# Kernel tuning notes

Hardware: AMD Instinct MI355X
Metric: run time of the kernel (lower is better)

Reference implementation:

```python
import jax, jax.numpy as jnp
import numpy as np

EMBED = 64
HEADS = 2
HDIM = EMBED // HEADS  # 32
IN_FEAT = 256
NODES = 3


def _lin(x, W, b=None):
    y = x @ W.T
    return y + b if b is not None else y


def setup_inputs() -> dict:
    key = jax.random.key(0)
    ks = jax.random.split(key, 24)
    B = 131072
    s = 0.05
    inp = {
        "spatial": jax.random.normal(ks[0], (B, IN_FEAT), jnp.float32),
        "genomic": jax.random.normal(ks[1], (B, IN_FEAT), jnp.float32),
        "temporal": jax.random.normal(ks[2], (B, IN_FEAT), jnp.float32),
        "adj_matrix": jnp.ones((B, NODES, NODES), jnp.float32),
        # modality projections (Linear(256,64))
        "Wsp": jax.random.normal(ks[3], (EMBED, IN_FEAT)) * s,
        "bsp": jnp.zeros((EMBED,)),
        "Wge": jax.random.normal(ks[4], (EMBED, IN_FEAT)) * s,
        "bge": jnp.zeros((EMBED,)),
        "Wtm": jax.random.normal(ks[5], (EMBED, IN_FEAT)) * s,
        "btm": jnp.zeros((EMBED,)),
        # GAT: W Linear(64,64,no bias), attention Linear(2*head_dim=64 -> 1, no bias)
        "gat_W": jax.random.normal(ks[6], (EMBED, EMBED)) * s,
        "gat_a": jax.random.normal(ks[7], (2 * HDIM,)) * s,
        # MultiheadAttention(64, 2)
        "in_w": jax.random.normal(ks[8], (3 * EMBED, EMBED)) * s,
        "in_b": jnp.zeros((3 * EMBED,)),
        "out_w": jax.random.normal(ks[9], (EMBED, EMBED)) * s,
        "out_b": jnp.zeros((EMBED,)),
        # LayerNorm(64)
        "ln_g": jnp.ones((EMBED,)),
        "ln_b": jnp.zeros((EMBED,)),
        # predictor 64->32->16->2
        "p1_w": jax.random.normal(ks[10], (32, EMBED)) * s,
        "p1_b": jnp.zeros((32,)),
        "p2_w": jax.random.normal(ks[11], (16, 32)) * s,
        "p2_b": jnp.zeros((16,)),
        "p3_w": jax.random.normal(ks[12], (2, 16)) * s,
        "p3_b": jnp.zeros((2,)),
    }
    return inp


def reference(spatial, genomic, temporal, adj_matrix,
              Wsp, bsp, Wge, bge, Wtm, btm,
              gat_W, gat_a, in_w, in_b, out_w, out_b,
              ln_g, ln_b, p1_w, p1_b, p2_w, p2_b, p3_w, p3_b):
    # Dropout layers are identity in eval mode.
    B = spatial.shape[0]
    sp = jax.nn.relu(_lin(spatial, Wsp, bsp))   # [B, 64]
    ge = jax.nn.relu(_lin(genomic, Wge, bge))
    tm = jax.nn.relu(_lin(temporal, Wtm, btm))
    x = jnp.stack([sp, ge, tm], axis=1)          # [B, 3, 64]

    # ---- GAT layer (dense attention over 3 nodes, 2 heads) ----
    h = _lin(x, gat_W).reshape(B, NODES, HEADS, HDIM)  # [B,3,H,D]
    # a . concat(h_i, h_j) decomposes into a1.h_i + a2.h_j
    e_i = jnp.einsum('bnhd,d->bnh', h, gat_a[:HDIM])
    e_j = jnp.einsum('bnhd,d->bnh', h, gat_a[HDIM:])
    e = e_i[:, :, None, :] + e_j[:, None, :, :]        # [B,3,3,H]
    e = jnp.where(e > 0, e, 0.2 * e)                    # LeakyReLU(0.2)
    e = jnp.where(adj_matrix[..., None] == 0, -1e9, e)
    alpha = jax.nn.softmax(e, axis=2)                   # softmax over j
    h_out = jnp.einsum('bijh,bjhd->bihd', alpha, h).reshape(B, NODES, EMBED)
    gat_pooled = h_out.mean(axis=1)                     # [B, 64]

    # ---- Cross-modal MHA + residual LayerNorm ----
    qkv = _lin(x, in_w, in_b)                           # [B,3,192]
    q, k, v = jnp.split(qkv, 3, axis=-1)
    def heads(t):
        return t.reshape(B, NODES, HEADS, HDIM).transpose(0, 2, 1, 3)
    q, k, v = heads(q), heads(k), heads(v)              # [B,H,3,D]
    sc = jnp.einsum('bhqd,bhkd->bhqk', q, k) / jnp.sqrt(jnp.float32(HDIM))
    attn = jax.nn.softmax(sc, axis=-1)
    o = jnp.einsum('bhqk,bhkd->bhqd', attn, v).transpose(0, 2, 1, 3).reshape(B, NODES, EMBED)
    attn_out = _lin(o, out_w, out_b)
    y = x + attn_out
    mu = y.mean(-1, keepdims=True)
    var = ((y - mu) ** 2).mean(-1, keepdims=True)
    y = (y - mu) / jnp.sqrt(var + 1e-5) * ln_g + ln_b
    cross_modal = y.mean(axis=1)                        # [B, 64]

    # ---- Predictor ----
    combined = gat_pooled + cross_modal
    z = jax.nn.relu(_lin(combined, p1_w, p1_b))
    z = jax.nn.relu(_lin(z, p2_w, p2_b))
    out = _lin(z, p3_w, p3_b)                           # [B, 2]
    return out[:, 0], out[:, 1]
```

## Files before the change

kernel.cpp:

```cpp
#include <hip/hip_runtime.h>

typedef __attribute__((ext_vector_type(8))) short v8s;
typedef __attribute__((ext_vector_type(4))) float v4f;

#define MFMA16(a, b, c) __builtin_amdgcn_mfma_f32_16x16x32_bf16((a), (b), (c), 0, 0, 0)

__device__ __forceinline__ short f2bf(float f) {
    unsigned u = __float_as_uint(f);
    u += 0x7FFFu + ((u >> 16) & 1u);
    return (short)(u >> 16);
}
__device__ __forceinline__ float bf2f(short s) {
    return __uint_as_float(((unsigned)(unsigned short)s) << 16);
}
__device__ __forceinline__ float bfly16(float v) {
#pragma unroll
    for (int m = 1; m < 16; m <<= 1) v += __shfl_xor(v, m);
    return v;
}

__global__ void giman_prep(const float* __restrict__ Wsp, const float* __restrict__ Wge,
                           const float* __restrict__ Wtm, const float* __restrict__ gatW,
                           const float* __restrict__ inw, const float* __restrict__ outw,
                           const float* __restrict__ p1w, const float* __restrict__ p2w,
                           const float* __restrict__ in_b, const float* __restrict__ out_b,
                           short* __restrict__ ws) {
    int idx = blockIdx.x * 256 + threadIdx.x;
    if (idx < 72192) {
        int j = idx & 7, l = (idx >> 3) & 63;
        int lr = l & 15, lc = ((l >> 4) << 3) + j;
        float val;
        if (idx < 49152) {
            const float* W; int off;
            if (idx < 16384)      { W = Wsp; off = idx; }
            else if (idx < 32768) { W = Wge; off = idx - 16384; }
            else                  { W = Wtm; off = idx - 32768; }
            int t = off >> 9, kk = t & 7, nb = t >> 3;
            val = W[(nb * 16 + lr) * 256 + kk * 32 + lc];
        } else if (idx < 53248) {
            int t = (idx - 49152) >> 9, kk = t & 1, nb = t >> 1;
            val = gatW[(nb * 16 + lr) * 64 + kk * 32 + lc];
        } else if (idx < 61440) {
            int t = (idx - 53248) >> 9, kk = t & 1, nb = t >> 1;
            val = inw[(nb * 16 + lr) * 64 + kk * 32 + lc];
        } else if (idx < 69632) {
            int t = (idx - 61440) >> 9, kk = t & 1, nbh = t >> 1;
            int h = nbh >> 2, nb = nbh & 3;
            int r = nb * 16 + lr, c = kk * 32 + lc;
            float s = 0.f;
            for (int k = 0; k < 32; ++k)
                s += outw[r * 64 + h * 32 + k] * inw[(128 + h * 32 + k) * 64 + c];
            val = s;
        } else if (idx < 71680) {
            int t = (idx - 69632) >> 9, kk = t & 1, nb = t >> 1;
            val = p1w[(nb * 16 + lr) * 64 + kk * 32 + lc];
        } else {
            val = p2w[lr * 32 + lc];
        }
        ws[idx] = f2bf(val);
    } else if (idx < 72256) {
        int r = idx - 72192;
        float s = out_b[r];
        for (int k = 0; k < 64; ++k) s += outw[r * 64 + 128 + k] * in_b[128 + k];
        ((float*)(ws + 72192))[r] = s;
    }
}

__global__ __launch_bounds__(256)
void giman_main(const float* __restrict__ spatial, const float* __restrict__ genomic,
                const float* __restrict__ temporal, const float* __restrict__ adj,
                const short* __restrict__ wf,
                const float* __restrict__ bsp, const float* __restrict__ bge,
                const float* __restrict__ btm, const float* __restrict__ gat_a,
                const float* __restrict__ in_b, const float* __restrict__ ln_g,
                const float* __restrict__ ln_b, const float* __restrict__ p1b,
                const float* __restrict__ p2b, const float* __restrict__ p3w,
                const float* __restrict__ p3bb,
                float* __restrict__ dout, int Btot)
{
    __shared__ __align__(16) short x_lds[4][48][72];
    __shared__ __align__(16) short c_lds[4][16][72];
    __shared__ __align__(16) float a_lds[4][148];

    const int wv   = threadIdx.x >> 6;
    const int lane = threadIdx.x & 63;
    const int lq   = lane & 15;
    const int lg   = lane >> 4;
    const int s0   = blockIdx.x * 64 + wv * 16;
    if (s0 + 16 > Btot) return;

    short (*xw)[72] = x_lds[wv];

    if (lane < 36)
        *(float4*)&a_lds[wv][lane * 4] = *(const float4*)(adj + (size_t)s0 * 9 + lane * 4);

    const float* cbp = (const float*)(wf + 72192);
    float a1v[4], a2v[4], cbv[4], lgv[4], lbv[4], ibv[8];
#pragma unroll
    for (int nb = 0; nb < 4; ++nb) {
        int c = nb * 16 + lq;
        a1v[nb] = gat_a[c & 31];
        a2v[nb] = gat_a[32 + (c & 31)];
        cbv[nb] = cbp[c];
        lgv[nb] = ln_g[c];
        lbv[nb] = ln_b[c];
    }
#pragma unroll
    for (int nb = 0; nb < 8; ++nb) ibv[nb] = in_b[nb * 16 + lq];
    const float inv3 = 1.f / 3.f;

    {
        const float* Xs[3] = {spatial, genomic, temporal};
        const float* Bs[3] = {bsp, bge, btm};
#pragma unroll
        for (int m = 0; m < 3; ++m) {
            const float* X = Xs[m] + (size_t)(s0 + lq) * 256 + lg * 8;
            const v8s* bwf = (const v8s*)(wf + m * 16384);
            v4f acc[4];
#pragma unroll
            for (int nb = 0; nb < 4; ++nb) acc[nb] = (v4f){0.f, 0.f, 0.f, 0.f};
#pragma unroll 4
            for (int kk = 0; kk < 8; ++kk) {
                float4 u = *(const float4*)(X + kk * 32);
                float4 v = *(const float4*)(X + kk * 32 + 4);
                v8s af;
                af[0] = f2bf(u.x); af[1] = f2bf(u.y); af[2] = f2bf(u.z); af[3] = f2bf(u.w);
                af[4] = f2bf(v.x); af[5] = f2bf(v.y); af[6] = f2bf(v.z); af[7] = f2bf(v.w);
#pragma unroll
                for (int nb = 0; nb < 4; ++nb)
                    acc[nb] = MFMA16(af, bwf[(nb * 8 + kk) * 64 + lane], acc[nb]);
            }
#pragma unroll
            for (int nb = 0; nb < 4; ++nb) {
                float bb = Bs[m][nb * 16 + lq];
#pragma unroll
                for (int r = 0; r < 4; ++r) {
                    float v = acc[nb][r] + bb;
                    v = v > 0.f ? v : 0.f;
                    xw[(lg * 4 + r) * 3 + m][nb * 16 + lq] = f2bf(v);
                }
            }
        }
    }

    const v8s* gwf = (const v8s*)(wf + 49152);
    const v8s* qkf = (const v8s*)(wf + 53248);
    const v8s* uf  = (const v8s*)(wf + 61440);

#pragma unroll 1
    for (int t = 0; t < 4; ++t) {
        int rn = lq & 3; rn = (rn == 3) ? 2 : rn;
        const short* xrp = xw[(t * 4 + (lq >> 2)) * 3 + rn];
        v8s xa0 = *(const v8s*)(xrp + lg * 8);
        v8s xa1 = *(const v8s*)(xrp + 32 + lg * 8);

        float gp[4];
        {
            v4f hacc[4];
#pragma unroll
            for (int nb = 0; nb < 4; ++nb) {
                v4f a = (v4f){0.f, 0.f, 0.f, 0.f};
                a = MFMA16(xa0, gwf[(nb * 2 + 0) * 64 + lane], a);
                a = MFMA16(xa1, gwf[(nb * 2 + 1) * 64 + lane], a);
                hacc[nb] = a;
            }
            float ei[3][2] = {}, ej[3][2] = {};
#pragma unroll
            for (int nb = 0; nb < 4; ++nb) {
                int h = nb >> 1;
#pragma unroll
                for (int n = 0; n < 3; ++n) {
                    ei[n][h] += hacc[nb][n] * a1v[nb];
                    ej[n][h] += hacc[nb][n] * a2v[nb];
                }
            }
#pragma unroll
            for (int n = 0; n < 3; ++n)
#pragma unroll
                for (int h = 0; h < 2; ++h) { ei[n][h] = bfly16(ei[n][h]); ej[n][h] = bfly16(ej[n][h]); }

            const float* amp = &a_lds[wv][(t * 4 + lg) * 9];
            float wj0[2] = {}, wj1[2] = {}, wj2[2] = {};
#pragma unroll
            for (int h = 0; h < 2; ++h)
#pragma unroll
                for (int i = 0; i < 3; ++i) {
                    float e0 = ei[i][h] + ej[0][h]; e0 = e0 > 0.f ? e0 : 0.2f * e0; if (amp[i * 3 + 0] == 0.f) e0 = -1e9f;
                    float e1 = ei[i][h] + ej[1][h]; e1 = e1 > 0.f ? e1 : 0.2f * e1; if (amp[i * 3 + 1] == 0.f) e1 = -1e9f;
                    float e2 = ei[i][h] + ej[2][h]; e2 = e2 > 0.f ? e2 : 0.2f * e2; if (amp[i * 3 + 2] == 0.f) e2 = -1e9f;
                    float mx = fmaxf(e0, fmaxf(e1, e2));
                    float q0 = __expf(e0 - mx), q1 = __expf(e1 - mx), q2 = __expf(e2 - mx);
                    float inv = 1.f / (q0 + q1 + q2);
                    wj0[h] += q0 * inv; wj1[h] += q1 * inv; wj2[h] += q2 * inv;
                }
#pragma unroll
            for (int nb = 0; nb < 4; ++nb) {
                int h = nb >> 1;
                gp[nb] = (wj0[h] * hacc[nb][0] + wj1[h] * hacc[nb][1] + wj2[h] * hacc[nb][2]) * inv3;
            }
        }

        float al[2][9];
#pragma unroll
        for (int h = 0; h < 2; ++h) {
            v4f q0, q1, k0, k1;
            {
                float b0 = ibv[2 * h], b1 = ibv[2 * h + 1];
                float b2 = ibv[4 + 2 * h], b3 = ibv[5 + 2 * h];
                q0 = (v4f){b0, b0, b0, b0};
                q1 = (v4f){b1, b1, b1, b1};
                k0 = (v4f){b2, b2, b2, b2};
                k1 = (v4f){b3, b3, b3, b3};
            }
            q0 = MFMA16(xa0, qkf[((2 * h) * 2 + 0) * 64 + lane], q0);
            q0 = MFMA16(xa1, qkf[((2 * h) * 2 + 1) * 64 + lane], q0);
            q1 = MFMA16(xa0, qkf[((2 * h + 1) * 2 + 0) * 64 + lane], q1);
            q1 = MFMA16(xa1, qkf[((2 * h + 1) * 2 + 1) * 64 + lane], q1);
            k0 = MFMA16(xa0, qkf[((4 + 2 * h) * 2 + 0) * 64 + lane], k0);
            k0 = MFMA16(xa1, qkf[((4 + 2 * h) * 2 + 1) * 64 + lane], k0);
            k1 = MFMA16(xa0, qkf[((5 + 2 * h) * 2 + 0) * 64 + lane], k1);
            k1 = MFMA16(xa1, qkf[((5 + 2 * h) * 2 + 1) * 64 + lane], k1);

            float s_[9];
#pragma unroll
            for (int i = 0; i < 3; ++i)
#pragma unroll
                for (int j = 0; j < 3; ++j)
                    s_[i * 3 + j] = bfly16(q0[i] * k0[j] + q1[i] * k1[j]);
#pragma unroll
            for (int i = 0; i < 3; ++i) {
                float e0 = s_[i * 3 + 0] * 0.17677669529663687f;
                float e1 = s_[i * 3 + 1] * 0.17677669529663687f;
                float e2 = s_[i * 3 + 2] * 0.17677669529663687f;
                float mx = fmaxf(e0, fmaxf(e1, e2));
                float w0 = __expf(e0 - mx), w1 = __expf(e1 - mx), w2 = __expf(e2 - mx);
                float inv = 1.f / (w0 + w1 + w2);
                al[h][i * 3 + 0] = w0 * inv;
                al[h][i * 3 + 1] = w1 * inv;
                al[h][i * 3 + 2] = w2 * inv;
            }
        }

        float y[4][3];
#pragma unroll
        for (int nb = 0; nb < 4; ++nb)
#pragma unroll
            for (int r = 0; r < 3; ++r)
                y[nb][r] = bf2f(xw[(t * 4 + lg) * 3 + r][nb * 16 + lq]) + cbv[nb];
#pragma unroll
        for (int h = 0; h < 2; ++h)
#pragma unroll
            for (int nb = 0; nb < 4; ++nb) {
                v4f u = (v4f){0.f, 0.f, 0.f, 0.f};
                u = MFMA16(xa0, uf[((h * 4 + nb) * 2 + 0) * 64 + lane], u);
                u = MFMA16(xa1, uf[((h * 4 + nb) * 2 + 1) * 64 + lane], u);
#pragma unroll
                for (int r = 0; r < 3; ++r)
                    y[nb][r] += al[h][r * 3 + 0] * u[0] + al[h][r * 3 + 1] * u[1]
                              + al[h][r * 3 + 2] * u[2];
            }

        float mu[3], rs[3];
#pragma unroll
        for (int r = 0; r < 3; ++r) {
            float sm = y[0][r] + y[1][r] + y[2][r] + y[3][r];
            float sq = y[0][r] * y[0][r] + y[1][r] * y[1][r]
                     + y[2][r] * y[2][r] + y[3][r] * y[3][r];
            sm = bfly16(sm); sq = bfly16(sq);
            float m_ = sm * (1.f / 64.f);
            float var = sq * (1.f / 64.f) - m_ * m_;
            mu[r] = m_;
            rs[r] = rsqrtf(var + 1e-5f);
        }
#pragma unroll
        for (int nb = 0; nb < 4; ++nb) {
            float cm = (y[nb][0] - mu[0]) * rs[0] + (y[nb][1] - mu[1]) * rs[1]
                     + (y[nb][2] - mu[2]) * rs[2];
            float comb = gp[nb] + cm * inv3 * lgv[nb] + lbv[nb];
            c_lds[wv][t * 4 + lg][nb * 16 + lq] = f2bf(comb);
        }
    }

    {
        const v8s* p1f = (const v8s*)(wf + 69632);
        const v8s* p2f = (const v8s*)(wf + 71680);
        short (*zw)[40] = (short (*)[40])(&x_lds[wv][0][0]);
        const short* crp = &c_lds[wv][lq][0];
        v8s ca0 = *(const v8s*)(crp + lg * 8);
        v8s ca1 = *(const v8s*)(crp + 32 + lg * 8);
        const float pb1v0 = p1b[lq], pb1v1 = p1b[16 + lq], pb2v = p2b[lq];
        const float p3w0 = p3w[lq], p3w1 = p3w[16 + lq];
        v4f z1[2];
#pragma unroll
        for (int nb = 0; nb < 2; ++nb) {
            float bb = nb ? pb1v1 : pb1v0;
            v4f a = (v4f){bb, bb, bb, bb};
            a = MFMA16(ca0, p1f[(nb * 2 + 0) * 64 + lane], a);
            a = MFMA16(ca1, p1f[(nb * 2 + 1) * 64 + lane], a);
            z1[nb] = a;
        }
#pragma unroll
        for (int nb = 0; nb < 2; ++nb)
#pragma unroll
            for (int r = 0; r < 4; ++r) {
                float v = z1[nb][r];
                v = v > 0.f ? v : 0.f;
                zw[lg * 4 + r][nb * 16 + lq] = f2bf(v);
            }
        v8s za = *(const v8s*)(&zw[lq][0] + lg * 8);
        v4f z2 = (v4f){pb2v, pb2v, pb2v, pb2v};
        z2 = MFMA16(za, p2f[lane], z2);
        const float p3b0 = p3bb[0], p3b1 = p3bb[1];
#pragma unroll
        for (int r = 0; r < 4; ++r) {
            float v = z2[r];
            v = v > 0.f ? v : 0.f;
            float po0 = bfly16(v * p3w0);
            float po1 = bfly16(v * p3w1);
            if (lq == 0) {
                dout[s0 + lg * 4 + r] = po0 + p3b0;
                dout[Btot + s0 + lg * 4 + r] = po1 + p3b1;
            }
        }
    }
}

extern "C" void kernel_launch(void* const* d_in, const int* in_sizes, int n_in,
                              void* d_out, int out_size, void* d_ws, size_t ws_size,
                              hipStream_t stream) {
    const float* spatial  = (const float*)d_in[0];
    const float* genomic  = (const float*)d_in[1];
    const float* temporal = (const float*)d_in[2];
    const float* adj      = (const float*)d_in[3];
    const float* Wsp = (const float*)d_in[4];
    const float* bsp = (const float*)d_in[5];
    const float* Wge = (const float*)d_in[6];
    const float* bge = (const float*)d_in[7];
    const float* Wtm = (const float*)d_in[8];
    const float* btm = (const float*)d_in[9];
    const float* gatW  = (const float*)d_in[10];
    const float* gat_a = (const float*)d_in[11];
    const float* in_w  = (const float*)d_in[12];
    const float* in_b  = (const float*)d_in[13];
    const float* out_w = (const float*)d_in[14];
    const float* out_b = (const float*)d_in[15];
    const float* ln_g  = (const float*)d_in[16];
    const float* ln_b  = (const float*)d_in[17];
    const float* p1w = (const float*)d_in[18];
    const float* p1b = (const float*)d_in[19];
    const float* p2w = (const float*)d_in[20];
    const float* p2b = (const float*)d_in[21];
    const float* p3w = (const float*)d_in[22];
    const float* p3b = (const float*)d_in[23];
    float* out = (float*)d_out;
    const int Btot = in_sizes[0] / 256;

    short* wf = (short*)d_ws;

    giman_prep<<<(72256 + 255) / 256, 256, 0, stream>>>(Wsp, Wge, Wtm, gatW, in_w, out_w,
                                                        p1w, p2w, in_b, out_b, wf);
    giman_main<<<Btot / 64, 256, 0, stream>>>(spatial, genomic, temporal, adj, wf,
                                              bsp, bge, btm, gat_a, in_b,
                                              ln_g, ln_b, p1b, p2b, p3w, p3b,
                                              out, Btot);
}
```

Before: 235.2 us.

## Fold GAT attention vector into weights and compute QK scores via MFMA

Precomputes gat_a·W as an extra MFMA weight block, so the GAT edge logits come out of two MFMAs plus shuffles instead of per-lane FMAs and butterfly reductions. The softmax scale is folded into the Q projection weights and bias. Q and K are staged through LDS and the 3x3 score matrix per head is produced with one MFMA instead of nine butterfly reductions. This adds LDS traffic and extra shared memory per block, which may lower occupancy, and rounds Q/K to bf16 before the score product.

```diff
diff --git a/kernel.cpp b/kernel.cpp
--- a/kernel.cpp
+++ b/kernel.cpp
@@ -4,6 +4,7 @@
 typedef __attribute__((ext_vector_type(4))) float v4f;
 
 #define MFMA16(a, b, c) __builtin_amdgcn_mfma_f32_16x16x32_bf16((a), (b), (c), 0, 0, 0)
+#define SCQ 0.17677669529663687f
 
 __device__ __forceinline__ short f2bf(float f) {
     unsigned u = __float_as_uint(f);
@@ -21,12 +22,13 @@
 
 __global__ void giman_prep(const float* __restrict__ Wsp, const float* __restrict__ Wge,
                            const float* __restrict__ Wtm, const float* __restrict__ gatW,
+                           const float* __restrict__ gat_a,
                            const float* __restrict__ inw, const float* __restrict__ outw,
                            const float* __restrict__ p1w, const float* __restrict__ p2w,
                            const float* __restrict__ in_b, const float* __restrict__ out_b,
                            short* __restrict__ ws) {
     int idx = blockIdx.x * 256 + threadIdx.x;
-    if (idx < 72192) {
+    if (idx < 73216) {
         int j = idx & 7, l = (idx >> 3) & 63;
         int lr = l & 15, lc = ((l >> 4) << 3) + j;
         float val;
@@ -37,32 +39,44 @@
             else                  { W = Wtm; off = idx - 32768; }
             int t = off >> 9, kk = t & 7, nb = t >> 3;
             val = W[(nb * 16 + lr) * 256 + kk * 32 + lc];
-        } else if (idx < 53248) {
+        } else if (idx < 54272) {
             int t = (idx - 49152) >> 9, kk = t & 1, nb = t >> 1;
-            val = gatW[(nb * 16 + lr) * 64 + kk * 32 + lc];
-        } else if (idx < 61440) {
-            int t = (idx - 53248) >> 9, kk = t & 1, nb = t >> 1;
-            val = inw[(nb * 16 + lr) * 64 + kk * 32 + lc];
-        } else if (idx < 69632) {
-            int t = (idx - 61440) >> 9, kk = t & 1, nbh = t >> 1;
+            if (nb < 4) {
+                val = gatW[(nb * 16 + lr) * 64 + kk * 32 + lc];
+            } else {
+                val = 0.f;
+                if (lr < 4) {
+                    int f = kk * 32 + lc;
+                    float s = 0.f;
+                    for (int d = 0; d < 32; ++d)
+                        s += gat_a[(lr >> 1) * 32 + d] * gatW[((lr & 1) * 32 + d) * 64 + f];
+                    val = s;
+                }
+            }
+        } else if (idx < 62464) {
+            int t = (idx - 54272) >> 9, kk = t & 1, nb = t >> 1;
+            int row = nb * 16 + lr;
+            val = inw[row * 64 + kk * 32 + lc] * (row < 64 ? SCQ : 1.f);
+        } else if (idx < 70656) {
+            int t = (idx - 62464) >> 9, kk = t & 1, nbh = t >> 1;
             int h = nbh >> 2, nb = nbh & 3;
             int r = nb * 16 + lr, c = kk * 32 + lc;
             float s = 0.f;
             for (int k = 0; k < 32; ++k)
                 s += outw[r * 64 + h * 32 + k] * inw[(128 + h * 32 + k) * 64 + c];
             val = s;
-        } else if (idx < 71680) {
-            int t = (idx - 69632) >> 9, kk = t & 1, nb = t >> 1;
+        } else if (idx < 72704) {
+            int t = (idx - 70656) >> 9, kk = t & 1, nb = t >> 1;
             val = p1w[(nb * 16 + lr) * 64 + kk * 32 + lc];
         } else {
             val = p2w[lr * 32 + lc];
         }
         ws[idx] = f2bf(val);
-    } else if (idx < 72256) {
-        int r = idx - 72192;
+    } else if (idx < 73280) {
+        int r = idx - 73216;
         float s = out_b[r];
         for (int k = 0; k < 64; ++k) s += outw[r * 64 + 128 + k] * in_b[128 + k];
-        ((float*)(ws + 72192))[r] = s;
+        ((float*)(ws + 73216))[r] = s;
     }
 }
 
@@ -71,7 +85,7 @@
                 const float* __restrict__ temporal, const float* __restrict__ adj,
                 const short* __restrict__ wf,
                 const float* __restrict__ bsp, const float* __restrict__ bge,
-                const float* __restrict__ btm, const float* __restrict__ gat_a,
+                const float* __restrict__ btm,
                 const float* __restrict__ in_b, const float* __restrict__ ln_g,
                 const float* __restrict__ ln_b, const float* __restrict__ p1b,
                 const float* __restrict__ p2b, const float* __restrict__ p3w,
@@ -80,33 +94,43 @@
 {
     __shared__ __align__(16) short x_lds[4][48][72];
     __shared__ __align__(16) short c_lds[4][16][72];
+    __shared__ __align__(16) short q_tr[4][16][72];
+    __shared__ __align__(16) short k_tr[4][16][72];
     __shared__ __align__(16) float a_lds[4][148];
 
     const int wv   = threadIdx.x >> 6;
     const int lane = threadIdx.x & 63;
     const int lq   = lane & 15;
     const int lg   = lane >> 4;
+    const int grpb = lane & 48;
     const int s0   = blockIdx.x * 64 + wv * 16;
     if (s0 + 16 > Btot) return;
 
     short (*xw)[72] = x_lds[wv];
+    short (*qtr)[72] = q_tr[wv];
+    short (*ktr)[72] = k_tr[wv];
 
     if (lane < 36)
         *(float4*)&a_lds[wv][lane * 4] = *(const float4*)(adj + (size_t)s0 * 9 + lane * 4);
 
-    const float* cbp = (const float*)(wf + 72192);
-    float a1v[4], a2v[4], cbv[4], lgv[4], lbv[4], ibv[8];
+#pragma unroll
+    for (int nb = 0; nb < 4; ++nb) {
+        qtr[lg * 4 + 3][nb * 16 + lq] = 0;
+        ktr[lg * 4 + 3][nb * 16 + lq] = 0;
+    }
+
+    const float* cbp = (const float*)(wf + 73216);
+    float cbv[4], lgv[4], lbv[4], ibv[8];
 #pragma unroll
     for (int nb = 0; nb < 4; ++nb) {
         int c = nb * 16 + lq;
-        a1v[nb] = gat_a[c & 31];
-        a2v[nb] = gat_a[32 + (c & 31)];
         cbv[nb] = cbp[c];
         lgv[nb] = ln_g[c];
         lbv[nb] = ln_b[c];
     }
 #pragma unroll
-    for (int nb = 0; nb < 8; ++nb) ibv[nb] = in_b[nb * 16 + lq];
+    for (int nb = 0; nb < 8; ++nb)
+        ibv[nb] = in_b[nb * 16 + lq] * (nb < 4 ? SCQ : 1.f);
     const float inv3 = 1.f / 3.f;
 
     {
@@ -144,8 +168,8 @@
     }
 
     const v8s* gwf = (const v8s*)(wf + 49152);
-    const v8s* qkf = (const v8s*)(wf + 53248);
-    const v8s* uf  = (const v8s*)(wf + 61440);
+    const v8s* qkf = (const v8s*)(wf + 54272);
+    const v8s* uf  = (const v8s*)(wf + 62464);
 
 #pragma unroll 1
     for (int t = 0; t < 4; ++t) {
@@ -164,20 +188,19 @@
                 a = MFMA16(xa1, gwf[(nb * 2 + 1) * 64 + lane], a);
                 hacc[nb] = a;
             }
-            float ei[3][2] = {}, ej[3][2] = {};
-#pragma unroll
-            for (int nb = 0; nb < 4; ++nb) {
-                int h = nb >> 1;
-#pragma unroll
-                for (int n = 0; n < 3; ++n) {
-                    ei[n][h] += hacc[nb][n] * a1v[nb];
-                    ej[n][h] += hacc[nb][n] * a2v[nb];
-                }
-            }
-#pragma unroll
-            for (int n = 0; n < 3; ++n)
-#pragma unroll
-                for (int h = 0; h < 2; ++h) { ei[n][h] = bfly16(ei[n][h]); ej[n][h] = bfly16(ej[n][h]); }
+            v4f eacc = (v4f){0.f, 0.f, 0.f, 0.f};
+            eacc = MFMA16(xa0, gwf[8 * 64 + lane], eacc);
+            eacc = MFMA16(xa1, gwf[9 * 64 + lane], eacc);
+
+            float eiv[3][2], ejv[3][2];
+#pragma unroll
+            for (int r = 0; r < 3; ++r) {
+#pragma unroll
+                for (int h = 0; h < 2; ++h) {
+                    eiv[r][h] = __shfl(eacc[r], grpb + h);
+                    ejv[r][h] = __shfl(eacc[r], grpb + 2 + h);
+                }
+            }
 
             const float* amp = &a_lds[wv][(t * 4 + lg) * 9];
             float wj0[2] = {}, wj1[2] = {}, wj2[2] = {};
@@ -185,9 +208,9 @@
             for (int h = 0; h < 2; ++h)
 #pragma unroll
                 for (int i = 0; i < 3; ++i) {
-                    float e0 = ei[i][h] + ej[0][h]; e0 = e0 > 0.f ? e0 : 0.2f * e0; if (amp[i * 3 + 0] == 0.f) e0 = -1e9f;
-                    float e1 = ei[i][h] + ej[1][h]; e1 = e1 > 0.f ? e1 : 0.2f * e1; if (amp[i * 3 + 1] == 0.f) e1 = -1e9f;
-                    float e2 = ei[i][h] + ej[2][h]; e2 = e2 > 0.f ? e2 : 0.2f * e2; if (amp[i * 3 + 2] == 0.f) e2 = -1e9f;
+                    float e0 = eiv[i][h] + ejv[0][h]; e0 = e0 > 0.f ? e0 : 0.2f * e0; if (amp[i * 3 + 0] == 0.f) e0 = -1e9f;
+                    float e1 = eiv[i][h] + ejv[1][h]; e1 = e1 > 0.f ? e1 : 0.2f * e1; if (amp[i * 3 + 1] == 0.f) e1 = -1e9f;
+                    float e2 = eiv[i][h] + ejv[2][h]; e2 = e2 > 0.f ? e2 : 0.2f * e2; if (amp[i * 3 + 2] == 0.f) e2 = -1e9f;
                     float mx = fmaxf(e0, fmaxf(e1, e2));
                     float q0 = __expf(e0 - mx), q1 = __expf(e1 - mx), q2 = __expf(e2 - mx);
                     float inv = 1.f / (q0 + q1 + q2);
@@ -200,44 +223,58 @@
             }
         }
 
+        {
+            v4f qa[4], ka[4];
+#pragma unroll
+            for (int nb = 0; nb < 4; ++nb) {
+                float bb = ibv[nb];
+                v4f a = (v4f){bb, bb, bb, bb};
+                a = MFMA16(xa0, qkf[(nb * 2 + 0) * 64 + lane], a);
+                a = MFMA16(xa1, qkf[(nb * 2 + 1) * 64 + lane], a);
+                qa[nb] = a;
+            }
+#pragma unroll
+            for (int nb = 0; nb < 4; ++nb) {
+                float bb = ibv[4 + nb];
+                v4f a = (v4f){bb, bb, bb, bb};
+                a = MFMA16(xa0, qkf[((4 + nb) * 2 + 0) * 64 + lane], a);
+                a = MFMA16(xa1, qkf[((4 + nb) * 2 + 1) * 64 + lane], a);
+                ka[nb] = a;
+            }
+#pragma unroll
+            for (int nb = 0; nb < 4; ++nb)
+#pragma unroll
+                for (int r = 0; r < 3; ++r) {
+                    qtr[lg * 4 + r][nb * 16 + lq] = f2bf(qa[nb][r]);
+                    ktr[lg * 4 + r][nb * 16 + lq] = f2bf(ka[nb][r]);
+                }
+        }
+
         float al[2][9];
-#pragma unroll
-        for (int h = 0; h < 2; ++h) {
-            v4f q0, q1, k0, k1;
-            {
-                float b0 = ibv[2 * h], b1 = ibv[2 * h + 1];
-                float b2 = ibv[4 + 2 * h], b3 = ibv[5 + 2 * h];
-                q0 = (v4f){b0, b0, b0, b0};
-                q1 = (v4f){b1, b1, b1, b1};
-                k0 = (v4f){b2, b2, b2, b2};
-                k1 = (v4f){b3, b3, b3, b3};
-            }
-            q0 = MFMA16(xa0, qkf[((2 * h) * 2 + 0) * 64 + lane], q0);
-            q0 = MFMA16(xa1, qkf[((2 * h) * 2 + 1) * 64 + lane], q0);
-            q1 = MFMA16(xa0, qkf[((2 * h + 1) * 2 + 0) * 64 + lane], q1);
-            q1 = MFMA16(xa1, qkf[((2 * h + 1) * 2 + 1) * 64 + lane], q1);
-            k0 = MFMA16(xa0, qkf[((4 + 2 * h) * 2 + 0) * 64 + lane], k0);
-            k0 = MFMA16(xa1, qkf[((4 + 2 * h) * 2 + 1) * 64 + lane], k0);
-            k1 = MFMA16(xa0, qkf[((5 + 2 * h) * 2 + 0) * 64 + lane], k1);
-            k1 = MFMA16(xa1, qkf[((5 + 2 * h) * 2 + 1) * 64 + lane], k1);
-
-            float s_[9];
-#pragma unroll
-            for (int i = 0; i < 3; ++i)
-#pragma unroll
-                for (int j = 0; j < 3; ++j)
-                    s_[i * 3 + j] = bfly16(q0[i] * k0[j] + q1[i] * k1[j]);
-#pragma unroll
-            for (int i = 0; i < 3; ++i) {
-                float e0 = s_[i * 3 + 0] * 0.17677669529663687f;
-                float e1 = s_[i * 3 + 1] * 0.17677669529663687f;
-                float e2 = s_[i * 3 + 2] * 0.17677669529663687f;
-                float mx = fmaxf(e0, fmaxf(e1, e2));
-                float w0 = __expf(e0 - mx), w1 = __expf(e1 - mx), w2 = __expf(e2 - mx);
-                float inv = 1.f / (w0 + w1 + w2);
-                al[h][i * 3 + 0] = w0 * inv;
-                al[h][i * 3 + 1] = w1 * inv;
-                al[h][i * 3 + 2] = w2 * inv;
+        {
+            const int sb = grpb + (grpb >> 2);
+#pragma unroll
+            for (int h = 0; h < 2; ++h) {
+                v8s aq = *(const v8s*)&qtr[lq][h * 32 + lg * 8];
+                v8s bk = *(const v8s*)&ktr[lq][h * 32 + lg * 8];
+                v4f S = (v4f){0.f, 0.f, 0.f, 0.f};
+                S = MFMA16(aq, bk, S);
+                float sc[9];
+#pragma unroll
+                for (int i = 0; i < 3; ++i)
+#pragma unroll
+                    for (int j = 0; j < 3; ++j)
+                        sc[i * 3 + j] = __shfl(S[i], sb + j);
+#pragma unroll
+                for (int i = 0; i < 3; ++i) {
+                    float e0 = sc[i * 3 + 0], e1 = sc[i * 3 + 1], e2 = sc[i * 3 + 2];
+                    float mx = fmaxf(e0, fmaxf(e1, e2));
+                    float w0 = __expf(e0 - mx), w1 = __expf(e1 - mx), w2 = __expf(e2 - mx);
+                    float inv = 1.f / (w0 + w1 + w2);
+                    al[h][i * 3 + 0] = w0 * inv;
+                    al[h][i * 3 + 1] = w1 * inv;
+                    al[h][i * 3 + 2] = w2 * inv;
+                }
             }
         }
 
@@ -282,8 +319,8 @@
     }
 
     {
-        const v8s* p1f = (const v8s*)(wf + 69632);
-        const v8s* p2f = (const v8s*)(wf + 71680);
+        const v8s* p1f = (const v8s*)(wf + 70656);
+        const v8s* p2f = (const v8s*)(wf + 72704);
         short (*zw)[40] = (short (*)[40])(&x_lds[wv][0][0]);
         const short* crp = &c_lds[wv][lq][0];
         v8s ca0 = *(const v8s*)(crp + lg * 8);
@@ -357,10 +394,11 @@
 
     short* wf = (short*)d_ws;
 
-    giman_prep<<<(72256 + 255) / 256, 256, 0, stream>>>(Wsp, Wge, Wtm, gatW, in_w, out_w,
-                                                        p1w, p2w, in_b, out_b, wf);
+    giman_prep<<<(73280 + 255) / 256, 256, 0, stream>>>(Wsp, Wge, Wtm, gatW, gat_a,
+                                                        in_w, out_w, p1w, p2w,
+                                                        in_b, out_b, wf);
     giman_main<<<Btot / 64, 256, 0, stream>>>(spatial, genomic, temporal, adj, wf,
-                                              bsp, bge, btm, gat_a, in_b,
+                                              bsp, bge, btm, in_b,
                                               ln_g, ln_b, p1b, p2b, p3w, p3b,
                                               out, Btot);
 }
```

Result: faster. 207.7 us (-11.7%).
